# Kernel tuning notes

Measured on AMD Instinct MI355X. Metric: run time of the kernel, lower is better.

## Reference

```python
import jax, jax.numpy as jnp
import numpy as np

BATCH = 16384
NNZ = 524288
INPUT_DIM = 30000
OUTPUT_DIM = 300


def setup_inputs() -> dict:
    key = jax.random.key(0)
    k1, k2, k3, k4 = jax.random.split(key, 4)
    sp_rows = jnp.sort(jax.random.randint(k1, (NNZ,), 0, BATCH, dtype=jnp.int32))
    sp_cols = jax.random.randint(k2, (NNZ,), 0, INPUT_DIM, dtype=jnp.int32)
    sp_vals = jax.random.uniform(k3, (NNZ,), dtype=jnp.float32)
    # glorot init for weights, zeros bias (as in the TF module)
    scale = jnp.sqrt(6.0 / (INPUT_DIM + OUTPUT_DIM)).astype(jnp.float32)
    weights = jax.random.uniform(k4, (INPUT_DIM, OUTPUT_DIM), dtype=jnp.float32,
                                 minval=-scale, maxval=scale)
    bias = jnp.zeros((OUTPUT_DIM,), dtype=jnp.float32)
    return {"sp_rows": sp_rows, "sp_cols": sp_cols, "sp_vals": sp_vals,
            "weights": weights, "bias": bias, "batch_size": BATCH}


def reference(sp_rows, sp_cols, sp_vals, weights, bias, batch_size):
    # sparse [batch, input_dim] @ dense [input_dim, output_dim]:
    # gather weight rows per nnz, scale by value, segment-sum into output rows.
    contrib = sp_vals[:, None] * weights[sp_cols]          # [nnz, output_dim]
    dense_vector = jax.ops.segment_sum(contrib, sp_rows,
                                       num_segments=batch_size)  # [batch, output_dim]
    dense_vector = dense_vector + bias
    return jax.nn.relu(dense_vector)
```

## Files before the change

kernel.cpp:

```cpp
#include <hip/hip_runtime.h>

#define OUT_DIM 300

typedef _Float16 half4_t __attribute__((ext_vector_type(4)));
typedef _Float16 half2_t __attribute__((ext_vector_type(2)));

__global__ __launch_bounds__(256) void row_ptr_scatter(
    const int* __restrict__ rows, int* __restrict__ row_ptr, int nnz, int batch)
{
    int i = blockIdx.x * 256 + threadIdx.x;
    if (i >= nnz) return;
    int r = rows[i];
    int prev = (i == 0) ? -1 : rows[i - 1];
    for (int q = prev + 1; q <= r; ++q) row_ptr[q] = i;
    if (i == nnz - 1)
        for (int q = r + 1; q <= batch; ++q) row_ptr[q] = nnz;
}

__global__ __launch_bounds__(256) void repack_f16_sliced(
    const float* __restrict__ w, unsigned char* __restrict__ wf, int in_dim)
{
    const int PPR = OUT_DIM / 2;
    int i = blockIdx.x * 256 + threadIdx.x;
    if (i >= in_dim * PPR) return;
    int row = i / PPR;
    int p   = i - row * PPR;
    int s   = p / 38;
    int pc  = p - s * 38;
    int stride = (s == 3) ? 144 : 152;
    size_t dst = (size_t)s * in_dim * 152 + (size_t)row * stride + (size_t)pc * 4;
    float2 f = *(const float2*)(w + (size_t)row * OUT_DIM + 2 * p);
    half2_t h;
    h.x = (_Float16)f.x;
    h.y = (_Float16)f.y;
    *(half2_t*)(wf + dst) = h;
}

__global__ __launch_bounds__(256) void spmm_sliced_f16(
    const int* __restrict__ row_ptr,
    const int* __restrict__ cols,
    const float* __restrict__ vals,
    const unsigned char* __restrict__ wf,
    const float* __restrict__ bias,
    float* __restrict__ out,
    int batch, int in_dim)
{
    const int slice = blockIdx.x & 3;
    const int wave  = threadIdx.x >> 6;
    const int lane  = threadIdx.x & 63;
    const int row   = (blockIdx.x >> 2) * 4 + wave;
    if (row >= batch) return;

    const int grp = lane >> 5;
    const int idx = lane & 31;

    const int nch    = (slice == 3) ? 18 : 19;
    const int stride = (slice == 3) ? 144 : 152;
    const size_t sbase = (size_t)slice * in_dim * 152;

    const unsigned char* wlane = wf + sbase + (size_t)idx * 8;

    const int lo = row_ptr[row];
    const int hi = row_ptr[row + 1];

    float4 acc = make_float4(0.f, 0.f, 0.f, 0.f);

    for (int base = lo; base < hi; base += 64) {
        const int rem = hi - base;
        const int cnt = rem < 64 ? rem : 64;

        int   off = 0;
        float v   = 0.0f;
        if (lane < cnt) {
            int c = cols[base + lane];
            v   = vals[base + lane];
            off = c * stride;
        }

        const int rounds = (cnt + 1) >> 1;
        const int rr = (rounds + 3) & ~3;
        for (int r = 0; r < rr; r += 4) {
#pragma unroll
            for (int u = 0; u < 4; ++u) {
                const int src = 2 * (r + u) + grp;
                const int   ob = __shfl(off, src);
                const float vb = __shfl(v,   src);
                half4_t wv = *(const half4_t*)(wlane + ob);
                acc.x = fmaf(vb, (float)wv.x, acc.x);
                acc.y = fmaf(vb, (float)wv.y, acc.y);
                acc.z = fmaf(vb, (float)wv.z, acc.z);
                acc.w = fmaf(vb, (float)wv.w, acc.w);
            }
        }
    }

    acc.x += __shfl_down(acc.x, 32);
    acc.y += __shfl_down(acc.y, 32);
    acc.z += __shfl_down(acc.z, 32);
    acc.w += __shfl_down(acc.w, 32);

    if (grp == 0 && idx < nch) {
        const int colb = 76 * slice + 4 * idx;
        const float4 b = *(const float4*)(bias + colb);
        float4 rv;
        rv.x = fmaxf(acc.x + b.x, 0.f);
        rv.y = fmaxf(acc.y + b.y, 0.f);
        rv.z = fmaxf(acc.z + b.z, 0.f);
        rv.w = fmaxf(acc.w + b.w, 0.f);
        *(float4*)(out + (size_t)row * OUT_DIM + colb) = rv;
    }
}

__global__ __launch_bounds__(256) void spmm_wave_f32_kernel(
    const int* __restrict__ row_ptr,
    const int* __restrict__ cols,
    const float* __restrict__ vals,
    const float* __restrict__ weights,
    const float* __restrict__ bias,
    float* __restrict__ out,
    int batch)
{
    const int wave = threadIdx.x >> 6;
    const int lane = threadIdx.x & 63;
    const int row  = blockIdx.x * 4 + wave;
    if (row >= batch) return;

    const int lo = row_ptr[row];
    const int hi = row_ptr[row + 1];

    float4 acc0 = make_float4(0.f, 0.f, 0.f, 0.f);
    float4 acc1 = make_float4(0.f, 0.f, 0.f, 0.f);
    const bool tail = (lane < 75 - 64);

    for (int base = lo; base < hi; base += 64) {
        const int rem = hi - base;
        const int cnt = rem < 64 ? rem : 64;
        int   c = 0;
        float v = 0.0f;
        if (lane < cnt) { c = cols[base + lane]; v = vals[base + lane]; }
        const int rounds = (cnt + 7) & ~7;
        for (int k = 0; k < rounds; k += 8) {
#pragma unroll
            for (int u = 0; u < 8; ++u) {
                const int   cc = __shfl(c, k + u);
                const float vv = __shfl(v, k + u);
                const float4* wrow = (const float4*)(weights + (size_t)cc * OUT_DIM);
                float4 w0 = wrow[lane];
                acc0.x += vv * w0.x; acc0.y += vv * w0.y;
                acc0.z += vv * w0.z; acc0.w += vv * w0.w;
                if (tail) {
                    float4 w1 = wrow[64 + lane];
                    acc1.x += vv * w1.x; acc1.y += vv * w1.y;
                    acc1.z += vv * w1.z; acc1.w += vv * w1.w;
                }
            }
        }
    }

    const float4* b4 = (const float4*)bias;
    float4* orow = (float4*)(out + (size_t)row * OUT_DIM);
    float4 b0 = b4[lane];
    float4 r0;
    r0.x = fmaxf(acc0.x + b0.x, 0.f);
    r0.y = fmaxf(acc0.y + b0.y, 0.f);
    r0.z = fmaxf(acc0.z + b0.z, 0.f);
    r0.w = fmaxf(acc0.w + b0.w, 0.f);
    orow[lane] = r0;
    if (tail) {
        float4 b1 = b4[64 + lane];
        float4 r1;
        r1.x = fmaxf(acc1.x + b1.x, 0.f);
        r1.y = fmaxf(acc1.y + b1.y, 0.f);
        r1.z = fmaxf(acc1.z + b1.z, 0.f);
        r1.w = fmaxf(acc1.w + b1.w, 0.f);
        orow[64 + lane] = r1;
    }
}

extern "C" void kernel_launch(void* const* d_in, const int* in_sizes, int n_in,
                              void* d_out, int out_size, void* d_ws, size_t ws_size,
                              hipStream_t stream) {
    const int*   sp_rows = (const int*)d_in[0];
    const int*   sp_cols = (const int*)d_in[1];
    const float* sp_vals = (const float*)d_in[2];
    const float* weights = (const float*)d_in[3];
    const float* bias    = (const float*)d_in[4];
    float* out = (float*)d_out;

    const int nnz    = in_sizes[0];
    const int w_elts = in_sizes[3];
    const int in_dim = w_elts / OUT_DIM;
    const int batch  = out_size / OUT_DIM;

    size_t rp_bytes = (size_t)(batch + 1) * sizeof(int);
    size_t wf_off   = (rp_bytes + 255) & ~(size_t)255;
    size_t need     = wf_off + (size_t)in_dim * 600 + 256;

    int* row_ptr = (int*)d_ws;

    row_ptr_scatter<<<(nnz + 255) / 256, 256, 0, stream>>>(
        sp_rows, row_ptr, nnz, batch);

    if (ws_size >= need) {
        unsigned char* wf = (unsigned char*)d_ws + wf_off;
        const int pairs = in_dim * (OUT_DIM / 2);
        repack_f16_sliced<<<(pairs + 255) / 256, 256, 0, stream>>>(
            weights, wf, in_dim);
        const int rowgroups = (batch + 3) / 4;
        spmm_sliced_f16<<<rowgroups * 4, 256, 0, stream>>>(
            row_ptr, sp_cols, sp_vals, wf, bias, out, batch, in_dim);
    } else {
        spmm_wave_f32_kernel<<<(batch + 3) / 4, 256, 0, stream>>>(
            row_ptr, sp_cols, sp_vals, weights, bias, out, batch);
    }
}
```

Before: 146.1 us.

## Process three nonzeros per wave round via LDS-broadcast offsets and padded slices

The sliced fp16 SpMM kernel now splits each 64-lane wave into three groups of nch lanes instead of two groups of 32. Each round therefore gathers three weight rows, where before it gathered two and left many lanes idle. Column offsets and values are staged in a per-wave shared-memory array rather than broadcast with shuffles, and the partial sums are reduced with two shuffle-downs. When the workspace is large enough, the repacked weight slices use a uniform 160-byte row stride. This may improve alignment but uses more workspace, and the spare lanes in the last group do redundant loads.

```diff
diff --git a/kernel.cpp b/kernel.cpp
--- a/kernel.cpp
+++ b/kernel.cpp
@@ -18,7 +18,8 @@
 }
 
 __global__ __launch_bounds__(256) void repack_f16_sliced(
-    const float* __restrict__ w, unsigned char* __restrict__ wf, int in_dim)
+    const float* __restrict__ w, unsigned char* __restrict__ wf,
+    int in_dim, int tierA)
 {
     const int PPR = OUT_DIM / 2;
     int i = blockIdx.x * 256 + threadIdx.x;
@@ -27,8 +28,9 @@
     int p   = i - row * PPR;
     int s   = p / 38;
     int pc  = p - s * 38;
-    int stride = (s == 3) ? 144 : 152;
-    size_t dst = (size_t)s * in_dim * 152 + (size_t)row * stride + (size_t)pc * 4;
+    int stride = tierA ? 160 : ((s == 3) ? 144 : 152);
+    size_t sbase = (size_t)s * in_dim * (tierA ? 160 : 152);
+    size_t dst = sbase + (size_t)row * stride + (size_t)pc * 4;
     float2 f = *(const float2*)(w + (size_t)row * OUT_DIM + 2 * p);
     half2_t h;
     h.x = (_Float16)f.x;
@@ -36,29 +38,32 @@
     *(half2_t*)(wf + dst) = h;
 }
 
-__global__ __launch_bounds__(256) void spmm_sliced_f16(
+__global__ __launch_bounds__(256) void spmm_sliced3(
     const int* __restrict__ row_ptr,
     const int* __restrict__ cols,
     const float* __restrict__ vals,
     const unsigned char* __restrict__ wf,
     const float* __restrict__ bias,
     float* __restrict__ out,
-    int batch, int in_dim)
-{
+    int batch, int in_dim, int tierA)
+{
+    __shared__ uint2 sh[4][76];
+
     const int slice = blockIdx.x & 3;
     const int wave  = threadIdx.x >> 6;
     const int lane  = threadIdx.x & 63;
     const int row   = (blockIdx.x >> 2) * 4 + wave;
     if (row >= batch) return;
 
-    const int grp = lane >> 5;
-    const int idx = lane & 31;
-
     const int nch    = (slice == 3) ? 18 : 19;
-    const int stride = (slice == 3) ? 144 : 152;
-    const size_t sbase = (size_t)slice * in_dim * 152;
-
-    const unsigned char* wlane = wf + sbase + (size_t)idx * 8;
+    const int stride = tierA ? 160 : ((slice == 3) ? 144 : 152);
+    const unsigned char* wslice = wf + (size_t)slice * in_dim * (tierA ? 160 : 152);
+
+    int grp = lane / nch;
+    int ch  = lane - grp * nch;
+    const int choff = ch * 8;
+
+    uint2* shw = sh[wave];
 
     const int lo = row_ptr[row];
     const int hi = row_ptr[row + 1];
@@ -69,44 +74,44 @@
         const int rem = hi - base;
         const int cnt = rem < 64 ? rem : 64;
 
-        int   off = 0;
-        float v   = 0.0f;
+        uint2 ov = make_uint2(0u, 0u);
         if (lane < cnt) {
             int c = cols[base + lane];
-            v   = vals[base + lane];
-            off = c * stride;
+            ov.x = (unsigned)(c * stride);
+            ov.y = __float_as_uint(vals[base + lane]);
         }
-
-        const int rounds = (cnt + 1) >> 1;
-        const int rr = (rounds + 3) & ~3;
-        for (int r = 0; r < rr; r += 4) {
+        shw[lane] = ov;
+        if (lane < 12) shw[64 + lane] = make_uint2(0u, 0u);
+
+        const int rr  = (cnt + 2) / 3;
+        const int rrp = (rr + 3) & ~3;
+        for (int r0 = 0; r0 < rrp; r0 += 4) {
 #pragma unroll
             for (int u = 0; u < 4; ++u) {
-                const int src = 2 * (r + u) + grp;
-                const int   ob = __shfl(off, src);
-                const float vb = __shfl(v,   src);
-                half4_t wv = *(const half4_t*)(wlane + ob);
-                acc.x = fmaf(vb, (float)wv.x, acc.x);
-                acc.y = fmaf(vb, (float)wv.y, acc.y);
-                acc.z = fmaf(vb, (float)wv.z, acc.z);
-                acc.w = fmaf(vb, (float)wv.w, acc.w);
+                uint2 q = shw[3 * (r0 + u) + grp];
+                float v = __uint_as_float(q.y);
+                half4_t wv = *(const half4_t*)(wslice + q.x + choff);
+                acc.x += v * (float)wv.x;
+                acc.y += v * (float)wv.y;
+                acc.z += v * (float)wv.z;
+                acc.w += v * (float)wv.w;
             }
         }
     }
 
-    acc.x += __shfl_down(acc.x, 32);
-    acc.y += __shfl_down(acc.y, 32);
-    acc.z += __shfl_down(acc.z, 32);
-    acc.w += __shfl_down(acc.w, 32);
-
-    if (grp == 0 && idx < nch) {
-        const int colb = 76 * slice + 4 * idx;
+    float ax = acc.x + __shfl_down(acc.x, nch) + __shfl_down(acc.x, 2 * nch);
+    float ay = acc.y + __shfl_down(acc.y, nch) + __shfl_down(acc.y, 2 * nch);
+    float az = acc.z + __shfl_down(acc.z, nch) + __shfl_down(acc.z, 2 * nch);
+    float aw = acc.w + __shfl_down(acc.w, nch) + __shfl_down(acc.w, 2 * nch);
+
+    if (lane < nch) {
+        const int colb = 76 * slice + 4 * lane;
         const float4 b = *(const float4*)(bias + colb);
         float4 rv;
-        rv.x = fmaxf(acc.x + b.x, 0.f);
-        rv.y = fmaxf(acc.y + b.y, 0.f);
-        rv.z = fmaxf(acc.z + b.z, 0.f);
-        rv.w = fmaxf(acc.w + b.w, 0.f);
+        rv.x = fmaxf(ax + b.x, 0.f);
+        rv.y = fmaxf(ay + b.y, 0.f);
+        rv.z = fmaxf(az + b.z, 0.f);
+        rv.w = fmaxf(aw + b.w, 0.f);
         *(float4*)(out + (size_t)row * OUT_DIM + colb) = rv;
     }
 }
@@ -194,21 +199,23 @@
 
     size_t rp_bytes = (size_t)(batch + 1) * sizeof(int);
     size_t wf_off   = (rp_bytes + 255) & ~(size_t)255;
-    size_t need     = wf_off + (size_t)in_dim * 600 + 256;
+    size_t needA    = wf_off + (size_t)in_dim * 640 + 256;
+    size_t needB    = wf_off + (size_t)in_dim * 600 + 256;
 
     int* row_ptr = (int*)d_ws;
 
     row_ptr_scatter<<<(nnz + 255) / 256, 256, 0, stream>>>(
         sp_rows, row_ptr, nnz, batch);
 
-    if (ws_size >= need) {
+    if (ws_size >= needB) {
+        const int tierA = (ws_size >= needA) ? 1 : 0;
         unsigned char* wf = (unsigned char*)d_ws + wf_off;
         const int pairs = in_dim * (OUT_DIM / 2);
         repack_f16_sliced<<<(pairs + 255) / 256, 256, 0, stream>>>(
-            weights, wf, in_dim);
+            weights, wf, in_dim, tierA);
         const int rowgroups = (batch + 3) / 4;
-        spmm_sliced_f16<<<rowgroups * 4, 256, 0, stream>>>(
-            row_ptr, sp_cols, sp_vals, wf, bias, out, batch, in_dim);
+        spmm_sliced3<<<rowgroups * 4, 256, 0, stream>>>(
+            row_ptr, sp_cols, sp_vals, wf, bias, out, batch, in_dim, tierA);
     } else {
         spmm_wave_f32_kernel<<<(batch + 3) / 4, 256, 0, stream>>>(
             row_ptr, sp_cols, sp_vals, weights, bias, out, batch);
```

New measurement: 140.0 us. 1.04x faster.
